# Performance work log

Hardware: AMD Instinct MI355X
Metric: run time of the kernel (lower is better)

## Reference

```python
import jax, jax.numpy as jnp
import numpy as np

D_MODEL = 1024
N_HEADS = 16
HEAD_DIM = D_MODEL // N_HEADS


def setup_inputs() -> dict:
    key = jax.random.key(0)
    k0, k1, k2, k3, k4, k5 = jax.random.split(key, 6)
    s = 1.0 / np.sqrt(D_MODEL)
    return {
        "q": jax.random.normal(k0, (2, 2048, D_MODEL), dtype=jnp.float32),
        "Wq": jax.random.normal(k1, (D_MODEL, D_MODEL), dtype=jnp.float32) * s,
        "Wk": jax.random.normal(k2, (D_MODEL, D_MODEL), dtype=jnp.float32) * s,
        "Wv": jax.random.normal(k3, (D_MODEL, D_MODEL), dtype=jnp.float32) * s,
        "Wo": jax.random.normal(k4, (D_MODEL, D_MODEL), dtype=jnp.float32) * s,
        "bo": jax.random.normal(k5, (D_MODEL,), dtype=jnp.float32) * 0.01,
    }


def _split_heads(x):
    b, s, _ = x.shape
    return x.reshape(b, s, N_HEADS, HEAD_DIM).transpose(0, 2, 1, 3)  # [b,h,s,d]


def reference(q, Wq, Wk, Wv, Wo, bo):
    # self-attention: k = v = q
    qh = _split_heads(q @ Wq)  # [b,h,s,d]
    kh = _split_heads(q @ Wk)
    vh = _split_heads(q @ Wv)
    scale = 1.0 / np.sqrt(HEAD_DIM).astype(np.float32)
    scores = jnp.einsum("bhqd,bhkd->bhqk", qh, kh) * scale
    attn = jax.nn.softmax(scores, axis=-1)
    ctx = jnp.einsum("bhqk,bhkd->bhqd", attn, vh)
    b, h, s, d = ctx.shape
    ctx = ctx.transpose(0, 2, 1, 3).reshape(b, s, h * d)
    return ctx @ Wo + bo
```

## Files before the change

kernel.cpp:

```cpp
#include <hip/hip_runtime.h>
#include <cstdint>

typedef unsigned short u16;
typedef __bf16 bf16x8 __attribute__((ext_vector_type(8)));
typedef __bf16 bf16x2 __attribute__((ext_vector_type(2)));
typedef float floatx4 __attribute__((ext_vector_type(4)));
typedef unsigned short u16x4 __attribute__((ext_vector_type(4)));
typedef unsigned short u16x8 __attribute__((ext_vector_type(8)));

#define MFMA16(a, b, c) __builtin_amdgcn_mfma_f32_16x16x32_bf16((a), (b), (c), 0, 0, 0)
#define QSCALE_LOG2E 0.18033688011112042f


typedef __attribute__((address_space(3))) void as3_void;
typedef __attribute__((address_space(1))) void as1_void;

static __device__ __forceinline__ void async_load16(const void* g, void* l) {
  __builtin_amdgcn_global_load_lds((as1_void*)(uintptr_t)g, (as3_void*)(uintptr_t)l,
                                   16, 0, 0);
}

static __device__ __forceinline__ u16 f2bf(float f) {
  union { float f; unsigned int u; } v; v.f = f;
  unsigned int u = v.u;
  u += 0x7fffu + ((u >> 16) & 1u);
  return (u16)(u >> 16);
}

static __device__ __forceinline__ u16x4 pack_bf4(float a, float b, float c, float d) {
#if __has_builtin(__builtin_amdgcn_cvt_pk_bf16_f32)
  union { u16x4 v4; bf16x2 v2[2]; } u;
  u.v2[0] = __builtin_amdgcn_cvt_pk_bf16_f32(a, b);
  u.v2[1] = __builtin_amdgcn_cvt_pk_bf16_f32(c, d);
  return u.v4;
#else
  u16x4 r; r[0] = f2bf(a); r[1] = f2bf(b); r[2] = f2bf(c); r[3] = f2bf(d);
  return r;
#endif
}

static __device__ __forceinline__ float fast_exp2(float x) {
#if __has_builtin(__builtin_amdgcn_exp2f)
  return __builtin_amdgcn_exp2f(x);
#else
  return exp2f(x);
#endif
}


__global__ __launch_bounds__(256) void prep_kernel(
    const float* __restrict__ w0, const float* __restrict__ w1,
    const float* __restrict__ w2, const float* __restrict__ w3,
    u16* __restrict__ wout,
    const float* __restrict__ xin, u16* __restrict__ xout) {
  if (blockIdx.z == 4) {
    int blk = blockIdx.y * 16 + blockIdx.x;
    size_t base = (size_t)blk * 16384 + (size_t)threadIdx.x * 8;
#pragma unroll
    for (int r = 0; r < 8; r++) {
      size_t i = base + (size_t)r * 2048;
      float4 a = *(const float4*)(xin + i);
      float4 b = *(const float4*)(xin + i + 4);
      u16x8 o;
      o[0] = f2bf(a.x); o[1] = f2bf(a.y); o[2] = f2bf(a.z); o[3] = f2bf(a.w);
      o[4] = f2bf(b.x); o[5] = f2bf(b.y); o[6] = f2bf(b.z); o[7] = f2bf(b.w);
      *(u16x8*)(xout + i) = o;
    }
    return;
  }
  __shared__ u16 t[64][65];
  const float* in = (blockIdx.z == 0) ? w0 : (blockIdx.z == 1) ? w1
                    : (blockIdx.z == 2) ? w2 : w3;
  u16* oz = wout + (size_t)blockIdx.z * (1024 * 1024);
  const int tid = threadIdx.x;
  const int x = tid & 63, y0 = tid >> 6;
  const int bx = blockIdx.x * 64, by = blockIdx.y * 64;
#pragma unroll
  for (int p = 0; p < 16; p++) {
    int y = y0 + p * 4;
    t[y][x] = f2bf(in[(size_t)(by + y) * 1024 + bx + x]);
  }
  __syncthreads();
#pragma unroll
  for (int p = 0; p < 16; p++) {
    int r = y0 + p * 4;
    oz[(size_t)(bx + r) * 1024 + by + x] = t[x][r];
  }
}


__global__ __launch_bounds__(256, 3) void gemm_bt_kernel(
    const u16* __restrict__ A, const u16* __restrict__ BT,
    const float* __restrict__ bias, void* __restrict__ out,
    u16* __restrict__ outVT,
    int M, int N, int K, int mode) {
  __shared__ u16 As[128 * 32];
  __shared__ u16 Bs[128 * 32];
  const int tid = threadIdx.x;
  const int w = tid >> 6, lane = tid & 63;
  const int bm = blockIdx.y * 128, bn = blockIdx.x * 128;
  const int z = blockIdx.z;
  const u16* Bz = BT + (size_t)z * N * K;

  const int c0 = w * 2, c1 = c0 + 1;
  const int mA0 = c0 * 16 + (lane >> 2), mA1 = c1 * 16 + (lane >> 2);
  const int kg0 = (lane & 3) ^ ((mA0 >> 1) & 3);
  const int kg1 = (lane & 3) ^ ((mA1 >> 1) & 3);
  const u16* agp0 = A + (size_t)(bm + mA0) * K + kg0 * 8;
  const u16* agp1 = A + (size_t)(bm + mA1) * K + kg1 * 8;
  const u16* bgp0 = Bz + (size_t)(bn + mA0) * K + kg0 * 8;
  const u16* bgp1 = Bz + (size_t)(bn + mA1) * K + kg1 * 8;
  u16* ald0 = As + c0 * 512; u16* ald1 = As + c1 * 512;
  u16* bld0 = Bs + c0 * 512; u16* bld1 = Bs + c1 * 512;

  const int wm = (w >> 1) * 64, wn = (w & 1) * 64;
  floatx4 acc[4][4] = {};

  int a_off[4], b_off[4];
#pragma unroll
  for (int i = 0; i < 4; i++) {
    int m = wm + i * 16 + (lane & 15);
    a_off[i] = m * 32 + (((lane >> 4) ^ ((m >> 1) & 3)) * 8);
    int n = wn + i * 16 + (lane & 15);
    b_off[i] = n * 32 + (((lane >> 4) ^ ((n >> 1) & 3)) * 8);
  }

  for (int k0 = 0; k0 < K; k0 += 32) {
    __syncthreads();
    async_load16(agp0 + k0, ald0);
    async_load16(agp1 + k0, ald1);
    async_load16(bgp0 + k0, bld0);
    async_load16(bgp1 + k0, bld1);
    __syncthreads();
    bf16x8 af[4], bf[4];
#pragma unroll
    for (int i = 0; i < 4; i++) af[i] = *(const bf16x8*)(As + a_off[i]);
#pragma unroll
    for (int j = 0; j < 4; j++) bf[j] = *(const bf16x8*)(Bs + b_off[j]);
#pragma unroll
    for (int i = 0; i < 4; i++)
#pragma unroll
      for (int j = 0; j < 4; j++)
        acc[i][j] = MFMA16(af[i], bf[j], acc[i][j]);
  }

  const int roff = (lane >> 4) * 4;
  const int coff = lane & 15;
  if (mode == 0) {
    if (z == 2) {
#pragma unroll
      for (int i = 0; i < 4; i++) {
        int r0 = bm + wm + i * 16 + roff;
        int b = r0 >> 11, s = r0 & 2047;
#pragma unroll
        for (int j = 0; j < 4; j++) {
          int c = bn + wn + j * 16 + coff;
          int h = c >> 6, d = c & 63;
          u16x4 pk = pack_bf4(acc[i][j][0], acc[i][j][1], acc[i][j][2], acc[i][j][3]);
          *(u16x4*)(outVT + ((size_t)(b * 16 + h) * 64 + d) * 2048 + s) = pk;
        }
      }
    } else {
      const float sc = (z == 0) ? QSCALE_LOG2E : 1.0f;
      u16* outz = (u16*)out + (size_t)z * M * N;
#pragma unroll
      for (int i = 0; i < 4; i++) {
        int r0 = bm + wm + i * 16 + roff;
#pragma unroll
        for (int j = 0; j < 4; j++) {
          int c = bn + wn + j * 16 + coff;
#pragma unroll
          for (int r = 0; r < 4; r++)
            outz[(size_t)(r0 + r) * N + c] = f2bf(acc[i][j][r] * sc);
        }
      }
    }
  } else {
    float* outf = (float*)out;
#pragma unroll
    for (int i = 0; i < 4; i++) {
      int r0 = bm + wm + i * 16 + roff;
#pragma unroll
      for (int j = 0; j < 4; j++) {
        int c = bn + wn + j * 16 + coff;
        float bv = bias[c];
#pragma unroll
        for (int r = 0; r < 4; r++)
          outf[(size_t)(r0 + r) * N + c] = acc[i][j][r] + bv;
      }
    }
  }
}


__global__ __launch_bounds__(256, 3) void attn_kernel(
    const u16* __restrict__ Q, const u16* __restrict__ Kx,
    const u16* __restrict__ VT, u16* __restrict__ ctx) {
  __shared__ u16 Ks[128 * 64];
  __shared__ u16 Vs[64 * 128];
  __shared__ u16 Ps[4][32 * 72];
  const int tid = threadIdx.x;
  const int w = tid >> 6, lane = tid & 63;
  const int bid = blockIdx.x;
  const int bh = (bid >> 7) * 8 + (bid & 7);
  const int q0 = ((bid >> 3) & 15) * 128;
  const int b = bh >> 4, h = bh & 15;
  const u16* Qh = Q + (size_t)b * 2048 * 1024 + h * 64;
  const u16* Kh = Kx + (size_t)b * 2048 * 1024 + h * 64;
  const u16* Vh = VT + (size_t)bh * 64 * 2048;

  const int qbase = q0 + w * 32;
  bf16x8 qf[2][2];
#pragma unroll
  for (int qt = 0; qt < 2; qt++)
#pragma unroll
    for (int ks = 0; ks < 2; ks++)
      qf[qt][ks] = *(const bf16x8*)(Qh + (size_t)(qbase + qt * 16 + (lane & 15)) * 1024 +
                                    ks * 32 + (lane >> 4) * 8);

  bf16x8 onesf;
#pragma unroll
  for (int i = 0; i < 8; i++) onesf[i] = (__bf16)1.0f;
  const floatx4 zero4 = {};

  const u16* kgp[4]; const u16* vgp[4];
  u16* kld[4]; u16* vld[4];
#pragma unroll
  for (int i = 0; i < 4; i++) {
    int c = w * 4 + i;
    int sl = c * 8 + (lane >> 3);
    int dg = (lane & 7) ^ (lane >> 3);
    kgp[i] = Kh + (size_t)sl * 1024 + dg * 8;
    kld[i] = Ks + c * 512;
    int dl = c * 4 + (lane >> 4);
    int sg = (lane & 15) ^ (dl & 15);
    vgp[i] = Vh + (size_t)dl * 2048 + sg * 8;
    vld[i] = Vs + c * 512;
  }

  const int slot_k0 = (lane >> 4) ^ (lane & 7);
  const int slot_k1 = (4 + (lane >> 4)) ^ (lane & 7);
  const u16* kf0_base = Ks + (lane & 15) * 64 + slot_k0 * 8;
  const u16* kf1_base = Ks + (lane & 15) * 64 + slot_k1 * 8;

  floatx4 o[2][4] = {};
  floatx4 lacc[2] = {};
  u16* Pw = Ps[w];
  const int qrow0 = (lane & 15) * 72;
  const int qrow1 = (16 + (lane & 15)) * 72;
  const int quad = lane >> 4;

  for (int t = 0; t < 16; t++) {
    const int k0 = t * 128;
    __syncthreads();
#pragma unroll
    for (int i = 0; i < 4; i++) {
      async_load16(kgp[i] + (size_t)k0 * 1024, kld[i]);
      async_load16(vgp[i] + k0, vld[i]);
    }
    __syncthreads();

#pragma unroll
    for (int hh = 0; hh < 2; hh++) {
      floatx4 st0[4], st1[4];
#pragma unroll
      for (int si4 = 0; si4 < 4; si4++) {
        int si = hh * 4 + si4;
        bf16x8 kf0 = *(const bf16x8*)(kf0_base + si * 1024);
        bf16x8 kf1 = *(const bf16x8*)(kf1_base + si * 1024);
        st0[si4] = MFMA16(kf1, qf[0][1], MFMA16(kf0, qf[0][0], zero4));
        st1[si4] = MFMA16(kf1, qf[1][1], MFMA16(kf0, qf[1][0], zero4));
      }
#pragma unroll
      for (int si4 = 0; si4 < 4; si4++) {
        u16x4 pk0 = pack_bf4(fast_exp2(st0[si4][0]), fast_exp2(st0[si4][1]),
                             fast_exp2(st0[si4][2]), fast_exp2(st0[si4][3]));
        u16x4 pk1 = pack_bf4(fast_exp2(st1[si4][0]), fast_exp2(st1[si4][1]),
                             fast_exp2(st1[si4][2]), fast_exp2(st1[si4][3]));
        *(u16x4*)(Pw + qrow0 + si4 * 16 + quad * 4) = pk0;
        *(u16x4*)(Pw + qrow1 + si4 * 16 + quad * 4) = pk1;
      }
#pragma unroll
      for (int ksl = 0; ksl < 2; ksl++) {
        int kb = hh * 2 + ksl;
        bf16x8 vf[4];
#pragma unroll
        for (int jt = 0; jt < 4; jt++) {
          int d = jt * 16 + (lane & 15);
          int slot = (kb * 4 + quad) ^ (d & 15);
          vf[jt] = *(const bf16x8*)(Vs + d * 128 + slot * 8);
        }
#pragma unroll
        for (int qt = 0; qt < 2; qt++) {
          bf16x8 pf = *(const bf16x8*)(Pw + (qt * 16 + (lane & 15)) * 72 +
                                       ksl * 32 + quad * 8);
#pragma unroll
          for (int jt = 0; jt < 4; jt++)
            o[qt][jt] = MFMA16(pf, vf[jt], o[qt][jt]);
          lacc[qt] = MFMA16(pf, onesf, lacc[qt]);
        }
      }
    }
  }

#pragma unroll
  for (int qt = 0; qt < 2; qt++)
#pragma unroll
    for (int r = 0; r < 4; r++) {
      float inv = 1.0f / lacc[qt][r];
      int s = qbase + qt * 16 + quad * 4 + r;
#pragma unroll
      for (int j = 0; j < 4; j++) {
        int c = h * 64 + j * 16 + (lane & 15);
        ctx[(size_t)(b * 2048 + s) * 1024 + c] = f2bf(o[qt][j][r] * inv);
      }
    }
}


extern "C" void kernel_launch(void* const* d_in, const int* in_sizes, int n_in,
                              void* d_out, int out_size, void* d_ws, size_t ws_size,
                              hipStream_t stream) {
  (void)in_sizes; (void)n_in; (void)out_size; (void)ws_size;
  const float* x  = (const float*)d_in[0];
  const float* Wq = (const float*)d_in[1];
  const float* Wk = (const float*)d_in[2];
  const float* Wv = (const float*)d_in[3];
  const float* Wo = (const float*)d_in[4];
  const float* bo = (const float*)d_in[5];
  u16* ws = (u16*)d_ws;
  const size_t MM = 1024 * 1024;
  u16* WT  = ws;
  u16* WoT = ws + 3 * MM;
  u16* Xb  = ws + 4 * MM;
  u16* QKV = ws + 8 * MM;
  u16* VTp = ws + 20 * MM;
  u16* CTX = ws + 24 * MM;

  dim3 blk(256);
  prep_kernel<<<dim3(16, 16, 5), blk, 0, stream>>>(Wq, Wk, Wv, Wo, WT, x, Xb);
  gemm_bt_kernel<<<dim3(8, 32, 3), blk, 0, stream>>>(Xb, WT, nullptr, QKV, VTp,
                                                     4096, 1024, 1024, 0);
  attn_kernel<<<dim3(512, 1, 1), blk, 0, stream>>>(QKV, QKV + 4 * MM, VTp, CTX);
  gemm_bt_kernel<<<dim3(8, 32, 1), blk, 0, stream>>>(CTX, WoT, bo, d_out, nullptr,
                                                     4096, 1024, 1024, 1);
}
```

Before: 190.7 us.

## Stage V-transpose epilogue through LDS and split output GEMM into 128x64 tiles

The QKV GEMM is specialised, and for the V slice the accumulators are now staged through an LDS tile so the transposed V^T stores are written as coalesced 16-byte row segments instead of scattered 8-byte writes. The output projection moves to a dedicated kernel with 128x64 tiles, which doubles the block count to 512 so more of the GPU is filled for a GEMM that previously launched only 256 blocks. The narrower tile lowers reuse per block and adds extra barriers in the V epilogue.

```diff
diff --git a/kernel.cpp b/kernel.cpp
--- a/kernel.cpp
+++ b/kernel.cpp
@@ -89,17 +89,17 @@
 }
 
 
-__global__ __launch_bounds__(256, 3) void gemm_bt_kernel(
+__global__ __launch_bounds__(256, 3) void gemm_qkv_kernel(
     const u16* __restrict__ A, const u16* __restrict__ BT,
-    const float* __restrict__ bias, void* __restrict__ out,
-    u16* __restrict__ outVT,
-    int M, int N, int K, int mode) {
+    u16* __restrict__ out, u16* __restrict__ outVT) {
   __shared__ u16 As[128 * 32];
   __shared__ u16 Bs[128 * 32];
+  __shared__ u16 tb[64 * 136];
   const int tid = threadIdx.x;
   const int w = tid >> 6, lane = tid & 63;
   const int bm = blockIdx.y * 128, bn = blockIdx.x * 128;
   const int z = blockIdx.z;
+  const int K = 1024, N = 1024;
   const u16* Bz = BT + (size_t)z * N * K;
 
   const int c0 = w * 2, c1 = c0 + 1;
@@ -146,48 +146,127 @@
 
   const int roff = (lane >> 4) * 4;
   const int coff = lane & 15;
-  if (mode == 0) {
-    if (z == 2) {
-#pragma unroll
-      for (int i = 0; i < 4; i++) {
-        int r0 = bm + wm + i * 16 + roff;
-        int b = r0 >> 11, s = r0 & 2047;
-#pragma unroll
-        for (int j = 0; j < 4; j++) {
-          int c = bn + wn + j * 16 + coff;
-          int h = c >> 6, d = c & 63;
-          u16x4 pk = pack_bf4(acc[i][j][0], acc[i][j][1], acc[i][j][2], acc[i][j][3]);
-          *(u16x4*)(outVT + ((size_t)(b * 16 + h) * 64 + d) * 2048 + s) = pk;
+  if (z == 2) {
+    const int b = bm >> 11, s0 = bm & 2047;
+#pragma unroll
+    for (int half = 0; half < 2; half++) {
+      __syncthreads();
+      if ((w & 1) == half) {
+#pragma unroll
+        for (int i = 0; i < 4; i++) {
+          int s_local = wm + i * 16 + roff;
+#pragma unroll
+          for (int j = 0; j < 4; j++) {
+            int c_local = j * 16 + coff;
+            u16x4 pk = pack_bf4(acc[i][j][0], acc[i][j][1],
+                                acc[i][j][2], acc[i][j][3]);
+            *(u16x4*)(tb + c_local * 136 + s_local) = pk;
+          }
         }
       }
-    } else {
-      const float sc = (z == 0) ? QSCALE_LOG2E : 1.0f;
-      u16* outz = (u16*)out + (size_t)z * M * N;
-#pragma unroll
-      for (int i = 0; i < 4; i++) {
-        int r0 = bm + wm + i * 16 + roff;
-#pragma unroll
-        for (int j = 0; j < 4; j++) {
-          int c = bn + wn + j * 16 + coff;
-#pragma unroll
-          for (int r = 0; r < 4; r++)
-            outz[(size_t)(r0 + r) * N + c] = f2bf(acc[i][j][r] * sc);
-        }
+      __syncthreads();
+#pragma unroll
+      for (int p = 0; p < 4; p++) {
+        int c_local = (tid >> 4) & 15;
+        int row = p * 16 + c_local;
+        int so = tid & 15;
+        int cg = bn + half * 64 + row;
+        int h = cg >> 6, d = cg & 63;
+        u16x8 vv = *(const u16x8*)(tb + row * 136 + so * 8);
+        *(u16x8*)(outVT + ((size_t)(b * 16 + h) * 64 + d) * 2048 + s0 + so * 8) = vv;
       }
     }
   } else {
-    float* outf = (float*)out;
+    const float sc = (z == 0) ? QSCALE_LOG2E : 1.0f;
+    u16* outz = out + (size_t)z * 4096 * 1024;
 #pragma unroll
     for (int i = 0; i < 4; i++) {
       int r0 = bm + wm + i * 16 + roff;
 #pragma unroll
       for (int j = 0; j < 4; j++) {
         int c = bn + wn + j * 16 + coff;
-        float bv = bias[c];
 #pragma unroll
         for (int r = 0; r < 4; r++)
-          outf[(size_t)(r0 + r) * N + c] = acc[i][j][r] + bv;
-      }
+          outz[(size_t)(r0 + r) * N + c] = f2bf(acc[i][j][r] * sc);
+      }
+    }
+  }
+}
+
+
+__global__ __launch_bounds__(256, 2) void gemm_o_kernel(
+    const u16* __restrict__ A, const u16* __restrict__ BT,
+    const float* __restrict__ bias, float* __restrict__ out) {
+  __shared__ u16 As[128 * 32];
+  __shared__ u16 Bs[64 * 32];
+  const int tid = threadIdx.x;
+  const int w = tid >> 6, lane = tid & 63;
+  const int bm = blockIdx.y * 128, bn = blockIdx.x * 64;
+  const int K = 1024, N = 1024;
+
+  const u16* gp[3]; u16* ld[3];
+#pragma unroll
+  for (int i = 0; i < 3; i++) {
+    int c = w * 3 + i;
+    if (c < 8) {
+      int m = c * 16 + (lane >> 2);
+      int kg = (lane & 3) ^ ((m >> 1) & 3);
+      gp[i] = A + (size_t)(bm + m) * K + kg * 8;
+      ld[i] = As + c * 512;
+    } else {
+      int cb = c - 8;
+      int n = cb * 16 + (lane >> 2);
+      int kg = (lane & 3) ^ ((n >> 1) & 3);
+      gp[i] = BT + (size_t)(bn + n) * K + kg * 8;
+      ld[i] = Bs + cb * 512;
+    }
+  }
+
+  const int wm = (w >> 1) * 64, wn = (w & 1) * 32;
+  floatx4 acc[4][2] = {};
+
+  int a_off[4], b_off[2];
+#pragma unroll
+  for (int i = 0; i < 4; i++) {
+    int m = wm + i * 16 + (lane & 15);
+    a_off[i] = m * 32 + (((lane >> 4) ^ ((m >> 1) & 3)) * 8);
+  }
+#pragma unroll
+  for (int j = 0; j < 2; j++) {
+    int n = wn + j * 16 + (lane & 15);
+    b_off[j] = n * 32 + (((lane >> 4) ^ ((n >> 1) & 3)) * 8);
+  }
+
+  for (int k0 = 0; k0 < K; k0 += 32) {
+    __syncthreads();
+    async_load16(gp[0] + k0, ld[0]);
+    async_load16(gp[1] + k0, ld[1]);
+    async_load16(gp[2] + k0, ld[2]);
+    __syncthreads();
+    bf16x8 af[4], bf[2];
+#pragma unroll
+    for (int i = 0; i < 4; i++) af[i] = *(const bf16x8*)(As + a_off[i]);
+#pragma unroll
+    for (int j = 0; j < 2; j++) bf[j] = *(const bf16x8*)(Bs + b_off[j]);
+#pragma unroll
+    for (int i = 0; i < 4; i++)
+#pragma unroll
+      for (int j = 0; j < 2; j++)
+        acc[i][j] = MFMA16(af[i], bf[j], acc[i][j]);
+  }
+
+  const int roff = (lane >> 4) * 4;
+  const int coff = lane & 15;
+#pragma unroll
+  for (int i = 0; i < 4; i++) {
+    int r0 = bm + wm + i * 16 + roff;
+#pragma unroll
+    for (int j = 0; j < 2; j++) {
+      int c = bn + wn + j * 16 + coff;
+      float bv = bias[c];
+#pragma unroll
+      for (int r = 0; r < 4; r++)
+        out[(size_t)(r0 + r) * N + c] = acc[i][j][r] + bv;
     }
   }
 }
@@ -339,9 +418,7 @@
 
   dim3 blk(256);
   prep_kernel<<<dim3(16, 16, 5), blk, 0, stream>>>(Wq, Wk, Wv, Wo, WT, x, Xb);
-  gemm_bt_kernel<<<dim3(8, 32, 3), blk, 0, stream>>>(Xb, WT, nullptr, QKV, VTp,
-                                                     4096, 1024, 1024, 0);
+  gemm_qkv_kernel<<<dim3(8, 32, 3), blk, 0, stream>>>(Xb, WT, QKV, VTp);
   attn_kernel<<<dim3(512, 1, 1), blk, 0, stream>>>(QKV, QKV + 4 * MM, VTp, CTX);
-  gemm_bt_kernel<<<dim3(8, 32, 1), blk, 0, stream>>>(CTX, WoT, bo, d_out, nullptr,
-                                                     4096, 1024, 1024, 1);
-}
+  gemm_o_kernel<<<dim3(16, 32, 1), blk, 0, stream>>>(CTX, WoT, bo, (float*)d_out);
+}
```

After: 186.4 us. -2.3%, faster.
